# Performance work log

Hardware: AMD Instinct MI355X
Metric: run time of the kernel (lower is better)

Reference implementation:

```python
import jax, jax.numpy as jnp
import numpy as np

C = 512          # channels
G = 32           # GroupNorm groups (flax default)
H = 8            # num_heads
EPS = 1e-6       # GroupNorm epsilon (flax default)
SPATIAL = (64, 64)


def setup_inputs() -> dict:
    key = jax.random.key(0)
    k1, k2 = jax.random.split(key)
    x = jax.random.normal(k1, SPATIAL + (C,), dtype=jnp.float32)
    gn_scale = jnp.ones((C,), dtype=jnp.float32)
    gn_bias = jnp.zeros((C,), dtype=jnp.float32)
    w_qkv = jax.random.normal(k2, (C, 3 * C), dtype=jnp.float32) / np.sqrt(C)
    b_qkv = jnp.zeros((3 * C,), dtype=jnp.float32)
    return {"x": x, "gn_scale": gn_scale, "gn_bias": gn_bias,
            "w_qkv": w_qkv, "b_qkv": b_qkv}


def reference(x, gn_scale, gn_bias, w_qkv, b_qkv):
    spatial_shape = x.shape[:-1]
    T = int(np.prod(spatial_shape))
    xf = x.reshape(T, C)

    # GroupNorm over (all spatial positions, channels within group) per group
    xg = xf.reshape(T, G, C // G)
    mean = jnp.mean(xg, axis=(0, 2), keepdims=True)
    var = jnp.var(xg, axis=(0, 2), keepdims=True)
    xn = ((xg - mean) * jax.lax.rsqrt(var + EPS)).reshape(T, C)
    xn = xn * gn_scale + gn_bias

    # QKV projection; note strided split: reshape (T, 3C) -> (T, C, 3)
    qkv = (xn @ w_qkv + b_qkv).reshape(T, C, 3)
    q, k, v = qkv[..., 0], qkv[..., 1], qkv[..., 2]

    ch = C // H
    scale = 1.0 / np.sqrt(np.sqrt(ch))
    qh = (q * scale).reshape(T, H, ch)
    kh = (k * scale).reshape(T, H, ch)
    vh = v.reshape(T, H, ch)

    w = jnp.einsum('thc,shc->ths', qh, kh)      # (T, H, T) attention scores
    w = jax.nn.softmax(w, axis=-1)
    a = jnp.einsum('ths,shc->thc', w, vh)       # (T, H, ch)
    return a.reshape(spatial_shape + (C,))
```

## Files before the change

### kernel.cpp

```cpp
#include <hip/hip_runtime.h>
#include <hip/hip_bf16.h>
#include <stdint.h>

typedef __attribute__((ext_vector_type(8))) short bf16x8;
typedef __attribute__((ext_vector_type(4))) float f32x4;
typedef __attribute__((ext_vector_type(16))) float f32x16;
typedef unsigned short u16;
typedef unsigned int u32;

constexpr int T  = 4096;
constexpr int C  = 512;
constexpr int H  = 8;
constexpr int CH = 64;
constexpr float EPS = 1e-6f;
constexpr float QKS   = 0.35355339059327378f;
constexpr float QKS_Q = 0.35355339059327378f * 1.4426950408889634f;

__device__ __forceinline__ float bf2f(u16 u) {
    union { unsigned int i; float f; } v; v.i = ((unsigned int)u) << 16; return v.f;
}
__device__ __forceinline__ u16 f2bf(float f) {
    union { float f; unsigned int i; } v; v.f = f;
    return (u16)((v.i + 0x7FFFu + ((v.i >> 16) & 1u)) >> 16);
}
__device__ __forceinline__ u32 pk2bf(float a, float b) {
    __hip_bfloat162 h = __float22bfloat162_rn(make_float2(a, b));
    u32 r; __builtin_memcpy(&r, &h, 4); return r;
}
__device__ __forceinline__ float ldin(const void* p, int i, int f32) {
    return f32 ? ((const float*)p)[i] : bf2f(((const u16*)p)[i]);
}
__device__ __forceinline__ void async16(const void* g, void* l) {
    __builtin_amdgcn_global_load_lds(
        (const __attribute__((address_space(1))) void*)g,
        (__attribute__((address_space(3))) void*)l,
        16, 0, 0);
}
__device__ __forceinline__ u32 pktrunc(float a, float b) {
    u32 ua = __float_as_uint(a), ub = __float_as_uint(b);
    return __builtin_amdgcn_perm(ub, ua, 0x07060302u);
}

__global__ void k_stats1(const void* x, float* gs2, int* flag) {
    int b = blockIdx.x, tid = threadIdx.x;
    int lane = tid & 63, w = tid >> 6;
    __shared__ int cnt;
    __shared__ float red[4][32][2];
    if (tid == 0) cnt = 0;
    __syncthreads();
    const u16* u = (const u16*)x;
    int huge = 0;
    for (int i = tid; i < 1024; i += 256) {
        float a = fabsf(bf2f(u[i]));
        if (!(a < 1e4f)) huge++;
    }
    if (huge) atomicAdd(&cnt, huge);
    __syncthreads();
    int f32 = (cnt >= 8) ? 1 : 0;
    if (b == 0 && tid == 0) *flag = f32;
    float s1 = 0.f, s2 = 0.f;
    if (f32) {
        const float4* xp = (const float4*)x + b * 4096;
        #pragma unroll
        for (int i = 0; i < 16; i++) {
            float4 v = xp[i * 256 + tid];
            s1 += (v.x + v.y) + (v.z + v.w);
            s2 += (v.x*v.x + v.y*v.y) + (v.z*v.z + v.w*v.w);
        }
        s1 += __shfl_xor(s1, 1); s2 += __shfl_xor(s2, 1);
        s1 += __shfl_xor(s1, 2); s2 += __shfl_xor(s2, 2);
        if ((lane & 3) == 0) {
            int gl = (lane >> 2) + 16 * (w & 1);
            red[w][gl][0] = s1; red[w][gl][1] = s2;
        }
        __syncthreads();
        if (tid < 32) {
            int g = tid, w0 = (g < 16) ? 0 : 1;
            gs2[b * 64 + g * 2]     = red[w0][g][0] + red[w0 + 2][g][0];
            gs2[b * 64 + g * 2 + 1] = red[w0][g][1] + red[w0 + 2][g][1];
        }
    } else {
        const uint4* xp = (const uint4*)x + b * 2048;
        #pragma unroll
        for (int i = 0; i < 8; i++) {
            uint4 v = xp[i * 256 + tid];
            float f[8] = { bf2f((u16)(v.x&0xffff)), bf2f((u16)(v.x>>16)),
                           bf2f((u16)(v.y&0xffff)), bf2f((u16)(v.y>>16)),
                           bf2f((u16)(v.z&0xffff)), bf2f((u16)(v.z>>16)),
                           bf2f((u16)(v.w&0xffff)), bf2f((u16)(v.w>>16)) };
            #pragma unroll
            for (int j = 0; j < 8; j++) { s1 += f[j]; s2 += f[j]*f[j]; }
        }
        s1 += __shfl_xor(s1, 1); s2 += __shfl_xor(s2, 1);
        if ((lane & 1) == 0) { red[w][lane >> 1][0] = s1; red[w][lane >> 1][1] = s2; }
        __syncthreads();
        if (tid < 32) {
            int g = tid;
            gs2[b * 64 + g * 2]     = red[0][g][0]+red[1][g][0]+red[2][g][0]+red[3][g][0];
            gs2[b * 64 + g * 2 + 1] = red[0][g][1]+red[1][g][1]+red[2][g][1]+red[3][g][1];
        }
    }
}

__global__ void k_fuse(const void* x, const float* __restrict__ gs2,
                       const void* gsc, const void* gbi, const void* wq,
                       u16* __restrict__ xn, u16* __restrict__ wt,
                       const int* __restrict__ flag) {
    int bx = blockIdx.x, tid = threadIdx.x;
    int f32 = *flag;
    if (bx < 1024) {
        __shared__ float sred[64];
        if (tid < 64) {
            float a0 = 0.f, a1 = 0.f, a2 = 0.f, a3 = 0.f;
            const float* p = gs2 + tid;
            #pragma unroll
            for (int b = 0; b < 32; b++) {
                a0 += p[(4*b + 0) * 64];
                a1 += p[(4*b + 1) * 64];
                a2 += p[(4*b + 2) * 64];
                a3 += p[(4*b + 3) * 64];
            }
            sred[tid] = (a0 + a1) + (a2 + a3);
        }
        __syncthreads();
        int idx = (bx * 256 + tid) * 8;
        int c = idx & (C - 1);
        int g = c >> 4;
        float mean = sred[2 * g] * (1.0f / 65536.0f);
        float var  = sred[2 * g + 1] * (1.0f / 65536.0f) - mean * mean;
        float rstd = rsqrtf(var + EPS);
        float v[8];
        if (f32) {
            float4 x0 = *(const float4*)((const float*)x + idx);
            float4 x1 = *(const float4*)((const float*)x + idx + 4);
            v[0]=x0.x; v[1]=x0.y; v[2]=x0.z; v[3]=x0.w;
            v[4]=x1.x; v[5]=x1.y; v[6]=x1.z; v[7]=x1.w;
        } else {
            uint4 u = *(const uint4*)((const u16*)x + idx);
            v[0]=bf2f((u16)(u.x&0xffff)); v[1]=bf2f((u16)(u.x>>16));
            v[2]=bf2f((u16)(u.y&0xffff)); v[3]=bf2f((u16)(u.y>>16));
            v[4]=bf2f((u16)(u.z&0xffff)); v[5]=bf2f((u16)(u.z>>16));
            v[6]=bf2f((u16)(u.w&0xffff)); v[7]=bf2f((u16)(u.w>>16));
        }
        float r[8];
        #pragma unroll
        for (int i = 0; i < 8; i++) {
            float a = rstd * ldin(gsc, c + i, f32);
            r[i] = v[i] * a + (ldin(gbi, c + i, f32) - mean * a);
        }
        uint4 o;
        o.x = pk2bf(r[0], r[1]); o.y = pk2bf(r[2], r[3]);
        o.z = pk2bf(r[4], r[5]); o.w = pk2bf(r[6], r[7]);
        *(uint4*)(xn + idx) = o;
    } else {
        __shared__ u16 Wl[48][64];
        int b = bx - 1024;
        int k0 = (b >> 5) * 64, c0 = (b & 31) * 48;
        #pragma unroll
        for (int it = 0; it < 3; it++) {
            int u_ = it * 256 + tid;
            int r = u_ / 12, cu = u_ % 12;
            int gi = (k0 + r) * 1536 + c0 + cu * 4;
            float v0, v1, v2, v3;
            if (f32) {
                float4 t4 = *(const float4*)((const float*)wq + gi);
                v0 = t4.x; v1 = t4.y; v2 = t4.z; v3 = t4.w;
            } else {
                uint2 t2 = *(const uint2*)((const u16*)wq + gi);
                v0 = bf2f((u16)(t2.x & 0xffff)); v1 = bf2f((u16)(t2.x >> 16));
                v2 = bf2f((u16)(t2.y & 0xffff)); v3 = bf2f((u16)(t2.y >> 16));
            }
            Wl[cu*4+0][r] = f2bf(v0); Wl[cu*4+1][r] = f2bf(v1);
            Wl[cu*4+2][r] = f2bf(v2); Wl[cu*4+3][r] = f2bf(v3);
        }
        __syncthreads();
        #pragma unroll
        for (int it = 0; it < 2; it++) {
            int u_ = it * 256 + tid;
            if (u_ < 384) {
                int mrow = u_ >> 3, kc = u_ & 7;
                int j = mrow >> 4, cci = mrow & 15;
                int m = j * 512 + (c0 / 3) + cci;
                int cl = 3 * cci + j;
                uint4 val = *(const uint4*)&Wl[cl][kc * 8];
                *(uint4*)(wt + m * 512 + k0 + kc * 8) = val;
            }
        }
    }
}

__global__ __launch_bounds__(256) void k_gemm(
    const u16* __restrict__ xn, const u16* __restrict__ wt,
    const void* __restrict__ bq, const int* __restrict__ flag,
    u16* __restrict__ qh, u16* __restrict__ kh, u16* __restrict__ vt)
{
    __shared__ char smem[49152];
    u16* Al = (u16*)smem;
    u16* Bl = (u16*)(smem + 16384);
    int bx = blockIdx.x;
    int bm = bx & 63, bn = bx >> 6;
    int tid = threadIdx.x;
    int w = tid >> 6, lane = tid & 63, quad = lane >> 4, l15 = lane & 15;
    f32x4 acc[4][2] = {};
    const u16* Ag = xn + bm * 64 * 512;
    const u16* Bg = wt + bn * 128 * 512;

    #pragma unroll
    for (int i = 0; i < 2; i++) {
        int L = i * 256 + tid, row = L >> 3, cc = ((L & 7) ^ (row & 7)) * 8;
        async16(Ag + row * 512 + cc, (void*)(Al + L * 8));
    }
    #pragma unroll
    for (int i = 0; i < 4; i++) {
        int L = i * 256 + tid, row = L >> 3, cc = ((L & 7) ^ (row & 7)) * 8;
        async16(Bg + row * 512 + cc, (void*)(Bl + L * 8));
    }

    #pragma unroll
    for (int ki = 0; ki < 8; ki++) {
        __syncthreads();
        if (ki < 7) {
            int kn = (ki + 1) * 64;
            int bo = ((ki + 1) & 1);
            #pragma unroll
            for (int i = 0; i < 2; i++) {
                int L = i * 256 + tid, row = L >> 3, cc = ((L & 7) ^ (row & 7)) * 8;
                async16(Ag + row * 512 + kn + cc, (void*)(Al + bo * 4096 + L * 8));
            }
            #pragma unroll
            for (int i = 0; i < 4; i++) {
                int L = i * 256 + tid, row = L >> 3, cc = ((L & 7) ^ (row & 7)) * 8;
                async16(Bg + row * 512 + kn + cc, (void*)(Bl + bo * 8192 + L * 8));
            }
        }
        const u16* Ab = Al + (ki & 1) * 4096;
        const u16* Bb = Bl + (ki & 1) * 8192;
        #pragma unroll
        for (int kk = 0; kk < 2; kk++) {
            bf16x8 af[4], bfr[2];
            #pragma unroll
            for (int mi = 0; mi < 4; mi++) {
                int row = mi * 16 + l15;
                af[mi] = *(const bf16x8*)(Ab + row * 64 + (((kk * 4 + quad) ^ (row & 7)) * 8));
            }
            #pragma unroll
            for (int ni = 0; ni < 2; ni++) {
                int row = w * 32 + ni * 16 + l15;
                bfr[ni] = *(const bf16x8*)(Bb + row * 64 + (((kk * 4 + quad) ^ (row & 7)) * 8));
            }
            #pragma unroll
            for (int mi = 0; mi < 4; mi++)
                #pragma unroll
                for (int ni = 0; ni < 2; ni++)
                    acc[mi][ni] = __builtin_amdgcn_mfma_f32_16x16x32_bf16(
                        af[mi], bfr[ni], acc[mi][ni], 0, 0, 0);
        }
    }
    int f32 = *flag;
    int t_base = bm * 64;
    int j = bn >> 2;
    if (j < 2) {
        u16* dst = j ? kh : qh;
        float s = j ? QKS : QKS_Q;
        #pragma unroll
        for (int ni = 0; ni < 2; ni++) {
            int n = bn * 128 + w * 32 + ni * 16 + l15;
            int r = n & 511, hh = r >> 6, cc = r & 63;
            float bias = ldin(bq, 3 * r + j, f32);
            #pragma unroll
            for (int mi = 0; mi < 4; mi++) {
                int tq = t_base + mi * 16 + quad * 4;
                #pragma unroll
                for (int rg = 0; rg < 4; rg++)
                    dst[(hh * T + tq + rg) * CH + cc] = f2bf((acc[mi][ni][rg] + bias) * s);
            }
        }
    } else {
        __syncthreads();
        u16* Tt = (u16*)smem;
        u16* Tw = Tt + w * 2048;
        int rbase = (bn - 8) * 128 + w * 32;
        int hh = rbase >> 6;
        #pragma unroll
        for (int ni = 0; ni < 2; ni++) {
            int r = rbase + ni * 16 + l15;
            float bias = ldin(bq, 3 * (r & 511) + 2, f32);
            int rl = ni * 16 + l15;
            #pragma unroll
            for (int mi = 0; mi < 4; mi++) {
                uint2 pv;
                pv.x = pk2bf(acc[mi][ni][0] + bias, acc[mi][ni][1] + bias);
                pv.y = pk2bf(acc[mi][ni][2] + bias, acc[mi][ni][3] + bias);
                int cs = (mi * 2 + (quad >> 1)) ^ (rl & 7);
                *(uint2*)((u32*)Tw + rl * 32 + cs * 4 + (quad & 1) * 2) = pv;
            }
        }
        int cc_hi = (w & 1) * 32;
        #pragma unroll
        for (int rr = 0; rr < 4; rr++) {
            int rl = rr * 8 + (lane >> 3);
            int g = lane & 7;
            int cA = (g & ~1) ^ (rl & 7);
            int cB = ((g & ~1) + 1) ^ (rl & 7);
            int ofs = (g & 1) * 4;
            uint2 a = *(const uint2*)(Tw + rl * 64 + cA * 8 + ofs);
            uint2 b = *(const uint2*)(Tw + rl * 64 + cB * 8 + ofs);
            *(uint4*)(vt + (hh * CH + cc_hi + rl) * T + t_base + g * 8) =
                make_uint4(a.x, a.y, b.x, b.y);
        }
    }
}

__global__ __launch_bounds__(256, 4) void k_attn(
    const u16* __restrict__ qh, const u16* __restrict__ kh,
    const u16* __restrict__ vt, u16* __restrict__ opart, float* __restrict__ ls)
{
    __shared__ char lds[32768];
    u16* K0 = (u16*)lds;
    u16* V0 = (u16*)(lds + 16384);
    int bx = blockIdx.x;
    int h = bx >> 8, qb = (bx >> 3) & 31, ks = bx & 7;
    int t0 = qb * 128;
    int tid = threadIdx.x;
    int w = tid >> 6, lane = tid & 63;
    int l31 = lane & 31, hi = lane >> 5;

    const u16* Kg = kh + (h * T + ks * 512) * CH;
    const u16* Vg = vt + h * CH * T + ks * 512;

    int L0 = tid,       r0 = L0 >> 3, c0 = ((L0 & 7) ^ (r0 & 7)) * 8;
    int L1 = 256 + tid, r1 = L1 >> 3, c1 = ((L1 & 7) ^ (r1 & 7)) * 8;
    const u16* kp0 = Kg + r0 * CH + c0;
    const u16* kp1 = Kg + r1 * CH + c1;
    const u16* vp0 = Vg + r0 * T + c0;
    const u16* vp1 = Vg + r1 * T + c1;

    int off[2][4];
    #pragma unroll
    for (int rt = 0; rt < 2; rt++)
        #pragma unroll
        for (int c = 0; c < 4; c++) {
            int row = rt * 32 + l31;
            off[rt][c] = row * 64 + (((2 * c + hi) ^ (row & 7)) * 8);
        }

    bf16x8 bq[4];
    {
        const u16* qrow = qh + (h * T + t0 + w * 32 + l31) * CH;
        #pragma unroll
        for (int ksi = 0; ksi < 4; ksi++)
            bq[ksi] = *(const bf16x8*)(qrow + ksi * 16 + hi * 8);
    }

    async16(kp0, (void*)(K0 + L0 * 8));
    async16(kp1, (void*)(K0 + L1 * 8));
    async16(vp0, (void*)(V0 + L0 * 8));
    async16(vp1, (void*)(V0 + L1 * 8));

    f32x16 o[2] = {};
    float lsum = 0.f;

    for (int kt = 0; kt < 8; kt++) {
        int par = (kt & 1) * 4096;
        const u16* Kc = K0 + par;
        const u16* Vc = V0 + par;
        __syncthreads();
        if (kt < 7) {
            int nx = ((kt + 1) & 1) * 4096;
            int ko = (kt + 1) * 64 * CH;
            int vo = (kt + 1) * 64;
            async16(kp0 + ko, (void*)(K0 + nx + L0 * 8));
            async16(kp1 + ko, (void*)(K0 + nx + L1 * 8));
            async16(vp0 + vo, (void*)(V0 + nx + L0 * 8));
            async16(vp1 + vo, (void*)(V0 + nx + L1 * 8));
        }
        f32x16 sa[2] = {};
        #pragma unroll
        for (int t = 0; t < 2; t++)
            #pragma unroll
            for (int ksi = 0; ksi < 4; ksi++) {
                bf16x8 aK = *(const bf16x8*)(Kc + off[t][ksi]);
                sa[t] = __builtin_amdgcn_mfma_f32_32x32x16_bf16(aK, bq[ksi], sa[t], 0, 0, 0);
            }
        u32 bp[4][4];
        #pragma unroll
        for (int t = 0; t < 2; t++) {
            float rs = 0.f;
            #pragma unroll
            for (int pi = 0; pi < 8; pi++) {
                float e0 = exp2f(sa[t][2 * pi]);
                float e1 = exp2f(sa[t][2 * pi + 1]);
                rs += e0 + e1;
                bp[2 * t + (pi >> 2)][pi & 3] = pktrunc(e0, e1);
            }
            lsum += rs;
        }
        #pragma unroll
        for (int dt = 0; dt < 2; dt++)
            #pragma unroll
            for (int kst = 0; kst < 4; kst++) {
                bf16x8 aV = *(const bf16x8*)(Vc + off[dt][kst]);
                bf16x8 bpv;
                __builtin_memcpy(&bpv, bp[kst], 16);
                o[dt] = __builtin_amdgcn_mfma_f32_32x32x16_bf16(aV, bpv, o[dt], 0, 0, 0);
            }
    }
    lsum += __shfl_xor(lsum, 32);

    __syncthreads();
    float* Sw = (float*)(lds + w * 6144);
    int qg = t0 + w * 32;
    int q2 = lane >> 1, half = lane & 1;
    #pragma unroll
    for (int dt = 0; dt < 2; dt++) {
        #pragma unroll
        for (int reg = 0; reg < 16; reg++) {
            int dl = (reg & 3) + 8 * (reg >> 2) + 4 * hi;
            Sw[l31 * 33 + dl] = o[dt][reg];
        }
        const float* src = Sw + q2 * 33 + half * 16;
        u16* dst = opart + (size_t)((ks * 8 + h) * T + qg + q2) * 64 + dt * 32 + half * 16;
        u32 pk[8];
        #pragma unroll
        for (int i = 0; i < 8; i++) pk[i] = pk2bf(src[2 * i], src[2 * i + 1]);
        *(uint4*)(dst)     = make_uint4(pk[0], pk[1], pk[2], pk[3]);
        *(uint4*)(dst + 8) = make_uint4(pk[4], pk[5], pk[6], pk[7]);
    }
    if (hi == 0) ls[(ks * 8 + h) * T + qg + l31] = lsum;
}

__global__ void k_fin(const u16* __restrict__ opart, const float* __restrict__ ls,
                      void* __restrict__ out, const int* __restrict__ flag) {
    int idx = (blockIdx.x * 256 + threadIdx.x) * 8;
    int d0 = idx & 63;
    int ht = idx >> 6;
    int t = ht & (T - 1), h = ht >> 12;
    float lt = 0.f;
    #pragma unroll
    for (int s = 0; s < 8; s++) lt += ls[s * 32768 + ht];
    float inv = 1.0f / lt;
    float v[8] = {};
    #pragma unroll
    for (int s = 0; s < 8; s++) {
        uint4 a = *(const uint4*)(opart + s * 2097152 + idx);
        v[0] += bf2f((u16)(a.x & 0xffff)); v[1] += bf2f((u16)(a.x >> 16));
        v[2] += bf2f((u16)(a.y & 0xffff)); v[3] += bf2f((u16)(a.y >> 16));
        v[4] += bf2f((u16)(a.z & 0xffff)); v[5] += bf2f((u16)(a.z >> 16));
        v[6] += bf2f((u16)(a.w & 0xffff)); v[7] += bf2f((u16)(a.w >> 16));
    }
    #pragma unroll
    for (int i = 0; i < 8; i++) v[i] *= inv;
    int gbase = t * C + h * CH + d0;
    if (*flag) {
        *(float4*)((float*)out + gbase)     = make_float4(v[0], v[1], v[2], v[3]);
        *(float4*)((float*)out + gbase + 4) = make_float4(v[4], v[5], v[6], v[7]);
    } else {
        uint4 o;
        o.x = pk2bf(v[0], v[1]); o.y = pk2bf(v[2], v[3]);
        o.z = pk2bf(v[4], v[5]); o.w = pk2bf(v[6], v[7]);
        *(uint4*)((u16*)out + gbase) = o;
    }
}

extern "C" void kernel_launch(void* const* d_in, const int* in_sizes, int n_in,
                              void* d_out, int out_size, void* d_ws, size_t ws_size,
                              hipStream_t stream) {
    const void* x   = d_in[0];
    const void* gsc = d_in[1];
    const void* gbi = d_in[2];
    const void* wq  = d_in[3];
    const void* bq  = d_in[4];
    char* ws = (char*)d_ws;
    int*   flag = (int*)ws;
    char* base = ws + 8192;
    u16* qh = (u16*)(base);
    u16* kh = (u16*)(base + 4194304);
    u16* vt = (u16*)(base + 8388608);
    u16* xn = (u16*)(base + 12582912);
    u16* wt = (u16*)(base + 16777216);
    u16* opart = (u16*)(base + 12582912);
    float* ls    = (float*)(base + 46137344);
    float* gs2   = (float*)(base + 47185920);

    hipLaunchKernelGGL(k_stats1, dim3(128),  dim3(256), 0, stream, x, gs2, flag);
    hipLaunchKernelGGL(k_fuse,   dim3(1280), dim3(256), 0, stream, x, gs2, gsc, gbi, wq, xn, wt, flag);
    hipLaunchKernelGGL(k_gemm,   dim3(768),  dim3(256), 0, stream, xn, wt, bq, flag, qh, kh, vt);
    hipLaunchKernelGGL(k_attn,   dim3(2048), dim3(256), 0, stream, qh, kh, vt, opart, ls);
    hipLaunchKernelGGL(k_fin,    dim3(1024), dim3(256), 0, stream, opart, ls, d_out, flag);
}
```

Baseline: 157.2 us.

## Fold GroupNorm affine into QKV weights and bias, skip normalized-x pass

```diff
diff --git a/kernel.cpp b/kernel.cpp
--- a/kernel.cpp
+++ b/kernel.cpp
@@ -41,7 +41,7 @@
     return __builtin_amdgcn_perm(ub, ua, 0x07060302u);
 }
 
-__global__ void k_stats1(const void* x, float* gs2, int* flag) {
+__global__ void k_stats1(const void* x, float* gs2, int* flag, u16* xb, float* bacc) {
     int b = blockIdx.x, tid = threadIdx.x;
     int lane = tid & 63, w = tid >> 6;
     __shared__ int cnt;
@@ -58,6 +58,10 @@
     __syncthreads();
     int f32 = (cnt >= 8) ? 1 : 0;
     if (b == 0 && tid == 0) *flag = f32;
+    if (b == 0) {
+        #pragma unroll
+        for (int i = 0; i < 6; i++) bacc[i * 256 + tid] = 0.f;
+    }
     float s1 = 0.f, s2 = 0.f;
     if (f32) {
         const float4* xp = (const float4*)x + b * 4096;
@@ -66,6 +70,8 @@
             float4 v = xp[i * 256 + tid];
             s1 += (v.x + v.y) + (v.z + v.w);
             s2 += (v.x*v.x + v.y*v.y) + (v.z*v.z + v.w*v.w);
+            *(uint2*)(xb + (b * 4096 + i * 256 + tid) * 4) =
+                make_uint2(pk2bf(v.x, v.y), pk2bf(v.z, v.w));
         }
         s1 += __shfl_xor(s1, 1); s2 += __shfl_xor(s2, 1);
         s1 += __shfl_xor(s1, 2); s2 += __shfl_xor(s2, 2);
@@ -102,96 +108,86 @@
     }
 }
 
-__global__ void k_fuse(const void* x, const float* __restrict__ gs2,
-                       const void* gsc, const void* gbi, const void* wq,
-                       u16* __restrict__ xn, u16* __restrict__ wt,
+__global__ void k_prep(const float* __restrict__ gs2, const void* gsc, const void* gbi,
+                       const void* wq, u16* __restrict__ wt, float* __restrict__ bacc,
                        const int* __restrict__ flag) {
-    int bx = blockIdx.x, tid = threadIdx.x;
+    int b = blockIdx.x, tid = threadIdx.x;
     int f32 = *flag;
-    if (bx < 1024) {
-        __shared__ float sred[64];
-        if (tid < 64) {
-            float a0 = 0.f, a1 = 0.f, a2 = 0.f, a3 = 0.f;
-            const float* p = gs2 + tid;
-            #pragma unroll
-            for (int b = 0; b < 32; b++) {
-                a0 += p[(4*b + 0) * 64];
-                a1 += p[(4*b + 1) * 64];
-                a2 += p[(4*b + 2) * 64];
-                a3 += p[(4*b + 3) * 64];
-            }
-            sred[tid] = (a0 + a1) + (a2 + a3);
-        }
-        __syncthreads();
-        int idx = (bx * 256 + tid) * 8;
-        int c = idx & (C - 1);
-        int g = c >> 4;
-        float mean = sred[2 * g] * (1.0f / 65536.0f);
-        float var  = sred[2 * g + 1] * (1.0f / 65536.0f) - mean * mean;
+    int k0 = (b >> 5) * 64, c0 = (b & 31) * 48;
+    __shared__ float Alp[64], Bet[64];
+    __shared__ float sred2[2][8];
+    __shared__ u16 Wl[48][64];
+    float s[8] = {0,0,0,0,0,0,0,0};
+    if (tid < 128) {
+        const float* p = gs2 + tid * 64 + (k0 >> 4) * 2;
+        float4 aa = *(const float4*)p;
+        float4 bb = *(const float4*)(p + 4);
+        s[0]=aa.x; s[1]=aa.y; s[2]=aa.z; s[3]=aa.w;
+        s[4]=bb.x; s[5]=bb.y; s[6]=bb.z; s[7]=bb.w;
+    }
+    #pragma unroll
+    for (int off = 1; off < 64; off <<= 1)
+        #pragma unroll
+        for (int j = 0; j < 8; j++) s[j] += __shfl_xor(s[j], off);
+    if (tid < 128 && (tid & 63) == 0)
+        #pragma unroll
+        for (int j = 0; j < 8; j++) sred2[tid >> 6][j] = s[j];
+    __syncthreads();
+    if (tid < 64) {
+        int g = tid >> 4;
+        float S1 = sred2[0][g*2]     + sred2[1][g*2];
+        float S2 = sred2[0][g*2 + 1] + sred2[1][g*2 + 1];
+        float mean = S1 * (1.0f / 65536.0f);
+        float var  = S2 * (1.0f / 65536.0f) - mean * mean;
         float rstd = rsqrtf(var + EPS);
-        float v[8];
+        float a = rstd * ldin(gsc, k0 + tid, f32);
+        Alp[tid] = a;
+        Bet[tid] = ldin(gbi, k0 + tid, f32) - mean * a;
+    }
+    __syncthreads();
+    #pragma unroll
+    for (int it = 0; it < 3; it++) {
+        int u_ = it * 256 + tid;
+        int r = u_ / 12, cu = u_ % 12;
+        int gi = (k0 + r) * 1536 + c0 + cu * 4;
+        float v0, v1, v2, v3;
         if (f32) {
-            float4 x0 = *(const float4*)((const float*)x + idx);
-            float4 x1 = *(const float4*)((const float*)x + idx + 4);
-            v[0]=x0.x; v[1]=x0.y; v[2]=x0.z; v[3]=x0.w;
-            v[4]=x1.x; v[5]=x1.y; v[6]=x1.z; v[7]=x1.w;
+            float4 t4 = *(const float4*)((const float*)wq + gi);
+            v0 = t4.x; v1 = t4.y; v2 = t4.z; v3 = t4.w;
         } else {
-            uint4 u = *(const uint4*)((const u16*)x + idx);
-            v[0]=bf2f((u16)(u.x&0xffff)); v[1]=bf2f((u16)(u.x>>16));
-            v[2]=bf2f((u16)(u.y&0xffff)); v[3]=bf2f((u16)(u.y>>16));
-            v[4]=bf2f((u16)(u.z&0xffff)); v[5]=bf2f((u16)(u.z>>16));
-            v[6]=bf2f((u16)(u.w&0xffff)); v[7]=bf2f((u16)(u.w>>16));
-        }
-        float r[8];
-        #pragma unroll
-        for (int i = 0; i < 8; i++) {
-            float a = rstd * ldin(gsc, c + i, f32);
-            r[i] = v[i] * a + (ldin(gbi, c + i, f32) - mean * a);
-        }
-        uint4 o;
-        o.x = pk2bf(r[0], r[1]); o.y = pk2bf(r[2], r[3]);
-        o.z = pk2bf(r[4], r[5]); o.w = pk2bf(r[6], r[7]);
-        *(uint4*)(xn + idx) = o;
-    } else {
-        __shared__ u16 Wl[48][64];
-        int b = bx - 1024;
-        int k0 = (b >> 5) * 64, c0 = (b & 31) * 48;
-        #pragma unroll
-        for (int it = 0; it < 3; it++) {
-            int u_ = it * 256 + tid;
-            int r = u_ / 12, cu = u_ % 12;
-            int gi = (k0 + r) * 1536 + c0 + cu * 4;
-            float v0, v1, v2, v3;
-            if (f32) {
-                float4 t4 = *(const float4*)((const float*)wq + gi);
-                v0 = t4.x; v1 = t4.y; v2 = t4.z; v3 = t4.w;
-            } else {
-                uint2 t2 = *(const uint2*)((const u16*)wq + gi);
-                v0 = bf2f((u16)(t2.x & 0xffff)); v1 = bf2f((u16)(t2.x >> 16));
-                v2 = bf2f((u16)(t2.y & 0xffff)); v3 = bf2f((u16)(t2.y >> 16));
-            }
-            Wl[cu*4+0][r] = f2bf(v0); Wl[cu*4+1][r] = f2bf(v1);
-            Wl[cu*4+2][r] = f2bf(v2); Wl[cu*4+3][r] = f2bf(v3);
-        }
-        __syncthreads();
-        #pragma unroll
-        for (int it = 0; it < 2; it++) {
-            int u_ = it * 256 + tid;
-            if (u_ < 384) {
-                int mrow = u_ >> 3, kc = u_ & 7;
-                int j = mrow >> 4, cci = mrow & 15;
-                int m = j * 512 + (c0 / 3) + cci;
-                int cl = 3 * cci + j;
-                uint4 val = *(const uint4*)&Wl[cl][kc * 8];
-                *(uint4*)(wt + m * 512 + k0 + kc * 8) = val;
-            }
-        }
+            uint2 t2 = *(const uint2*)((const u16*)wq + gi);
+            v0 = bf2f((u16)(t2.x & 0xffff)); v1 = bf2f((u16)(t2.x >> 16));
+            v2 = bf2f((u16)(t2.y & 0xffff)); v3 = bf2f((u16)(t2.y >> 16));
+        }
+        float al = Alp[r];
+        Wl[cu*4+0][r] = f2bf(v0 * al); Wl[cu*4+1][r] = f2bf(v1 * al);
+        Wl[cu*4+2][r] = f2bf(v2 * al); Wl[cu*4+3][r] = f2bf(v3 * al);
+    }
+    __syncthreads();
+    #pragma unroll
+    for (int it = 0; it < 2; it++) {
+        int u_ = it * 256 + tid;
+        if (u_ < 384) {
+            int mrow = u_ >> 3, kc = u_ & 7;
+            int j = mrow >> 4, cci = mrow & 15;
+            int m = j * 512 + (c0 / 3) + cci;
+            int cl = 3 * cci + j;
+            *(uint4*)(wt + m * 512 + k0 + kc * 8) = *(const uint4*)&Wl[cl][kc * 8];
+        }
+    }
+    if (tid < 48) {
+        float acc = 0.f;
+        for (int k = 0; k < 64; k++)
+            acc += Bet[k] * ldin(wq, (k0 + k) * 1536 + c0 + tid, f32);
+        int col = c0 + tid, j = col % 3, cc = col / 3;
+        atomicAdd(&bacc[j * 512 + cc], acc);
     }
 }
 
 __global__ __launch_bounds__(256) void k_gemm(
-    const u16* __restrict__ xn, const u16* __restrict__ wt,
-    const void* __restrict__ bq, const int* __restrict__ flag,
+    const void* __restrict__ x, const u16* __restrict__ xb, const u16* __restrict__ wt,
+    const void* __restrict__ bq, const float* __restrict__ bacc,
+    const int* __restrict__ flag,
     u16* __restrict__ qh, u16* __restrict__ kh, u16* __restrict__ vt)
 {
     __shared__ char smem[49152];
@@ -201,8 +197,9 @@
     int bm = bx & 63, bn = bx >> 6;
     int tid = threadIdx.x;
     int w = tid >> 6, lane = tid & 63, quad = lane >> 4, l15 = lane & 15;
+    int f32 = *flag;
     f32x4 acc[4][2] = {};
-    const u16* Ag = xn + bm * 64 * 512;
+    const u16* Ag = (f32 ? xb : (const u16*)x) + bm * 64 * 512;
     const u16* Bg = wt + bn * 128 * 512;
 
     #pragma unroll
@@ -256,7 +253,6 @@
                         af[mi], bfr[ni], acc[mi][ni], 0, 0, 0);
         }
     }
-    int f32 = *flag;
     int t_base = bm * 64;
     int j = bn >> 2;
     if (j < 2) {
@@ -266,7 +262,7 @@
         for (int ni = 0; ni < 2; ni++) {
             int n = bn * 128 + w * 32 + ni * 16 + l15;
             int r = n & 511, hh = r >> 6, cc = r & 63;
-            float bias = ldin(bq, 3 * r + j, f32);
+            float bias = ldin(bq, 3 * r + j, f32) + bacc[n];
             #pragma unroll
             for (int mi = 0; mi < 4; mi++) {
                 int tq = t_base + mi * 16 + quad * 4;
@@ -284,7 +280,7 @@
         #pragma unroll
         for (int ni = 0; ni < 2; ni++) {
             int r = rbase + ni * 16 + l15;
-            float bias = ldin(bq, 3 * (r & 511) + 2, f32);
+            float bias = ldin(bq, 3 * (r & 511) + 2, f32) + bacc[1024 + (r & 511)];
             int rl = ni * 16 + l15;
             #pragma unroll
             for (int mi = 0; mi < 4; mi++) {
@@ -476,15 +472,16 @@
     u16* qh = (u16*)(base);
     u16* kh = (u16*)(base + 4194304);
     u16* vt = (u16*)(base + 8388608);
-    u16* xn = (u16*)(base + 12582912);
+    u16* xb = (u16*)(base + 12582912);
     u16* wt = (u16*)(base + 16777216);
     u16* opart = (u16*)(base + 12582912);
     float* ls    = (float*)(base + 46137344);
     float* gs2   = (float*)(base + 47185920);
-
-    hipLaunchKernelGGL(k_stats1, dim3(128),  dim3(256), 0, stream, x, gs2, flag);
-    hipLaunchKernelGGL(k_fuse,   dim3(1280), dim3(256), 0, stream, x, gs2, gsc, gbi, wq, xn, wt, flag);
-    hipLaunchKernelGGL(k_gemm,   dim3(768),  dim3(256), 0, stream, xn, wt, bq, flag, qh, kh, vt);
+    float* bacc  = (float*)(base + 47218688);
+
+    hipLaunchKernelGGL(k_stats1, dim3(128),  dim3(256), 0, stream, x, gs2, flag, xb, bacc);
+    hipLaunchKernelGGL(k_prep,   dim3(256),  dim3(256), 0, stream, gs2, gsc, gbi, wq, wt, bacc, flag);
+    hipLaunchKernelGGL(k_gemm,   dim3(768),  dim3(256), 0, stream, x, xb, wt, bq, bacc, flag, qh, kh, vt);
     hipLaunchKernelGGL(k_attn,   dim3(2048), dim3(256), 0, stream, qh, kh, vt, opart, ls);
     hipLaunchKernelGGL(k_fin,    dim3(1024), dim3(256), 0, stream, opart, ls, d_out, flag);
 }
```

New measurement: 158.5 us. No clear change (+0.9%).
